# Optimization experiments

Hardware: AMD Instinct MI355X
Metric: run time of the kernel (lower is better)

Reference implementation:

```python
import jax, jax.numpy as jnp
import numpy as np

NUM_BINS = 15
BW = 0.3                      # KDE bandwidth (hard-coded in original)
VOLUME = 100.0                # (-5,5) x (-5,5) integration volume
KDE_NORM = 2.0 * np.pi * BW * BW


def _sq_dists(q, data):
    # ||q_i - d_j||^2 via the algebraic expansion (avoids [Nq, Nd, 2] blowup)
    sq = (jnp.sum(q * q, axis=1)[:, None]
          + jnp.sum(data * data, axis=1)[None, :]
          - 2.0 * q @ data.T)
    return jnp.maximum(sq, 0.0)


def kde(data, q):
    # Gaussian KDE: sum_j exp(-||q-d_j||^2 / (2 bw^2)) / (n * 2*pi*bw^2)
    k = jnp.exp(-_sq_dists(q, data) / (2.0 * BW * BW))
    return jnp.sum(k, axis=1) / (data.shape[0] * KDE_NORM)


def kde_weighted(data, q, weights, count):
    # KDE restricted to the subset selected by `weights` (0/1 mask),
    # equivalent to kde(data[weights==1], q)
    k = jnp.exp(-_sq_dists(q, data) / (2.0 * BW * BW))
    return (k @ weights) / (jnp.maximum(count, 1.0) * KDE_NORM)


def setup_inputs() -> dict:
    key = jax.random.key(0)
    ks = jax.random.split(key, 10)
    B, NTR, NTE, NMC, NCLS = 1024, 20000, 10000, 10000, 10
    return {
        "batch_train_x": jax.random.normal(ks[0], (B, 2), jnp.float32),
        "batch_train_y": jax.random.randint(ks[1], (B,), 0, NCLS),
        "train_pred": jax.random.randint(ks[2], (B,), 0, NCLS),
        "train_probs": jax.random.uniform(ks[3], (NTR,), jnp.float32),
        "test_probs": jax.random.uniform(ks[4], (NTE,), jnp.float32),
        "train_x": jax.random.normal(ks[5], (NTR, 2), jnp.float32),
        "test_x": jax.random.normal(ks[6], (NTE, 2), jnp.float32),
        "W": jax.random.normal(ks[7], (2, NCLS), jnp.float32),
        "b": jax.random.normal(ks[8], (NCLS,), jnp.float32),
        "mc_points": jax.random.uniform(ks[9], (NUM_BINS, NMC, 2), jnp.float32,
                                        minval=-5.0, maxval=5.0),
    }


def reference(batch_train_x, batch_train_y, train_pred, train_probs,
              test_probs, W, b, train_x, test_x, mc_points):
    correct = (batch_train_y == train_pred)
    cw = correct.astype(jnp.float32)          # mask defining Xset_Y_hatY
    cnt = jnp.sum(cw)
    p_y_haty = cnt / batch_train_y.shape[0]   # P(Y == hatY)

    bins = jnp.linspace(0.0, 1.0, NUM_BINS + 1)
    lowers, uppers = bins[:-1], bins[1:]

    def body(ec, inp):
        lo, hi, x = inp                                    # x: [NMC, 2]
        tr_rate = jnp.mean(((train_probs > lo) & (train_probs <= hi)).astype(jnp.float32))
        te_rate = jnp.mean(((test_probs > lo) & (test_probs <= hi)).astype(jnp.float32))

        logits = x @ W + b
        hat_s = jax.lax.stop_gradient(jnp.max(jax.nn.softmax(logits, axis=1), axis=1))
        idx = ((hat_s >= lo) & (hat_s <= hi)).astype(x.dtype)

        kde_tr = kde(train_x, x)                           # reused twice
        safe_te = jnp.where(te_rate > 0, te_rate, 1.0)
        safe_tr = jnp.where(tr_rate > 0, tr_rate, 1.0)
        d_t = jnp.where(te_rate > 0, kde(test_x, x) / safe_te, 0.0) * idx
        d_s = jnp.where(tr_rate > 0, kde_tr / safe_tr, 0.0) * idx

        p_hs = kde_weighted(batch_train_x, x, cw, cnt) * p_y_haty / (kde_tr + 1e-8)
        p_hs = jnp.clip(p_hs, 0.0, 1.0)

        integral = jnp.mean(p_hs * (d_t - d_s)) * VOLUME   # MC integration
        ec = ec + jnp.where(te_rate > 0, te_rate * jnp.abs(integral), 0.0)
        return ec, None

    ec, _ = jax.lax.scan(body, jnp.float32(0.0), (lowers, uppers, mc_points))
    return ec
```

## Files before the change

kernel.cpp:

```cpp
#include <hip/hip_runtime.h>
#include <hip/hip_bf16.h>

#define NB    15
#define NMC   10000
#define NTR   20000
#define NTE   10000
#define BSZ   1024
#define NCLS  10
#define NQ_ALL (NB * NMC)

#define KDE_NORM  0.5654866776461628f
#define EXPC      8.014972449383130f
#define TWO_EXPC  16.029944898766260f
#define LOG2E     1.4426950408889634f

#define GX      12
#define NCELL   144
#define CELL_LO -6.0f

#define MC_ST  64
#define TR_ST  224
#define TE_ST  384
#define BX_ST  544
#define MC_CUR 704
#define TR_CUR 864
#define TE_CUR 1024
#define BX_CUR 1184
#define P_PR   1344
#define PR_ZERO_FLOATS (P_PR + 3 * NQ_ALL)
#define MCS_B   (PR_ZERO_FLOATS * 4)
#define TRS_B   (MCS_B + NQ_ALL * 16)
#define TES_B   (TRS_B + NTR * 16)
#define BXS_B   (TES_B + NTE * 16)
#define PR_NEED (BXS_B + BSZ * 16)

#define QCH    7
#define SLICES 16

#define CW_OFF   64
#define P_MID    1088
#define WS_MID_FLOATS (P_MID + 3 * NQ_ALL)
#define MDS   17
#define MTILE 256
#define MMQ   8

#define WS_SMALL 1088
#define FTILE 256

typedef float v2f __attribute__((ext_vector_type(2)));

__device__ __forceinline__ float fast_exp2(float x) {
#if __has_builtin(__builtin_amdgcn_exp2f)
    return __builtin_amdgcn_exp2f(x);
#else
    return exp2f(x);
#endif
}

__device__ __forceinline__ int cell_of(float x, float y) {
    int ix = (int)floorf(x - CELL_LO);
    ix = min(max(ix, 0), GX - 1);
    int iy = (int)floorf(y - CELL_LO);
    iy = min(max(iy, 0), GX - 1);
    return iy * GX + ix;
}

__global__ __launch_bounds__(1024) void setup_count_k(
    const int* __restrict__ by, const int* __restrict__ bp,
    const float* __restrict__ trp, const float* __restrict__ tep,
    const float2* __restrict__ mc, const float2* __restrict__ tr,
    const float2* __restrict__ te, const float2* __restrict__ bx,
    float* __restrict__ ws, int* __restrict__ W)
{
    __shared__ int h[4][NCELL];
    int tid = threadIdx.x;
    for (int s = tid; s < 4 * NCELL; s += 1024) ((int*)h)[s] = 0;
    __syncthreads();

    int i    = blockIdx.x * 1024 + tid;
    int lane = tid & 63;

    float c = 0.f;
    if (i < BSZ) c = (by[i] == bp[i]) ? 1.f : 0.f;
    unsigned long long mcm = __ballot(c != 0.f);
    if (lane == 0 && mcm) atomicAdd(&ws[0], (float)__popcll(mcm));

    if ((int)blockIdx.x * 1024 < NTR) {
        float p_tr = (i < NTR) ? trp[i] : -1.f;
        float p_te = (i < NTE) ? tep[i] : -1.f;
        const float step = 1.0f / 15.0f;
        for (int b2 = 0; b2 < NB; b2++) {
            float lo = b2 * step;
            float hi = (b2 == NB - 1) ? 1.0f : (b2 + 1) * step;
            unsigned long long m1 = __ballot(p_tr > lo && p_tr <= hi);
            unsigned long long m2 = __ballot(p_te > lo && p_te <= hi);
            if (lane == 0) {
                if (m1) atomicAdd(&ws[1  + b2], (float)__popcll(m1));
                if (m2) atomicAdd(&ws[16 + b2], (float)__popcll(m2));
            }
        }
    }

    if (i < NQ_ALL) { float2 p = mc[i]; atomicAdd(&h[0][cell_of(p.x, p.y)], 1); }
    if (i < NTR)    { float2 p = tr[i]; atomicAdd(&h[1][cell_of(p.x, p.y)], 1); }
    if (i < NTE)    { float2 p = te[i]; atomicAdd(&h[2][cell_of(p.x, p.y)], 1); }
    if (i < BSZ)    { float2 p = bx[i]; atomicAdd(&h[3][cell_of(p.x, p.y)], 1); }
    __syncthreads();

    for (int s = tid; s < 4 * NCELL; s += 1024) {
        int v = ((int*)h)[s];
        if (v) {
            int ds   = s / NCELL;
            int cell = s % NCELL;
            int st   = (ds == 0) ? MC_ST : (ds == 1) ? TR_ST : (ds == 2) ? TE_ST : BX_ST;
            atomicAdd(&W[st + 1 + cell], v);
        }
    }
}

__global__ void scan_k(int* __restrict__ W)
{
    __shared__ int buf[NCELL];
    int tid = threadIdx.x;
#pragma unroll
    for (int t = 0; t < 4; ++t) {
        int st  = (t == 0) ? MC_ST  : (t == 1) ? TR_ST  : (t == 2) ? TE_ST  : BX_ST;
        int cur = (t == 0) ? MC_CUR : (t == 1) ? TR_CUR : (t == 2) ? TE_CUR : BX_CUR;
        int v = 0;
        if (tid < NCELL) { v = W[st + 1 + tid]; buf[tid] = v; }
        __syncthreads();
        for (int off = 1; off < NCELL; off <<= 1) {
            int x = 0;
            if (tid < NCELL && tid >= off) x = buf[tid - off];
            __syncthreads();
            if (tid < NCELL) buf[tid] += x;
            __syncthreads();
        }
        if (tid < NCELL) {
            int start = buf[tid] - v;
            W[st  + tid] = start;
            W[cur + tid] = start;
            if (tid == NCELL - 1) W[st + NCELL] = buf[tid];
        }
        __syncthreads();
    }
}

__global__ __launch_bounds__(1024) void scatter_priv(
    const float2* __restrict__ mc, const float2* __restrict__ tr,
    const float2* __restrict__ te, const float2* __restrict__ bx,
    const int* __restrict__ by, const int* __restrict__ bp,
    int* __restrict__ W,
    float4* __restrict__ mcS, float4* __restrict__ trS,
    float4* __restrict__ teS, float4* __restrict__ bxS)
{
    __shared__ int h[NCELL];
    __shared__ int base[NCELL];
    int ds  = blockIdx.y;
    int N   = (ds == 0) ? NQ_ALL : (ds == 1) ? NTR : (ds == 2) ? NTE : BSZ;
    if ((int)blockIdx.x * 1024 >= N) return;
    const float2* src = (ds == 0) ? mc : (ds == 1) ? tr : (ds == 2) ? te : bx;
    int cur = (ds == 0) ? MC_CUR : (ds == 1) ? TR_CUR : (ds == 2) ? TE_CUR : BX_CUR;

    int tid = threadIdx.x;
    if (tid < NCELL) h[tid] = 0;
    __syncthreads();

    int i = blockIdx.x * 1024 + tid;
    int cell = 0, rank = 0;
    float2 p;
    if (i < N) {
        p = src[i];
        cell = cell_of(p.x, p.y);
        rank = atomicAdd(&h[cell], 1);
    }
    __syncthreads();
    if (tid < NCELL && h[tid]) base[tid] = atomicAdd(&W[cur + tid], h[tid]);
    __syncthreads();

    if (i < N) {
        int pos = base[cell] + rank;
        if (ds == 0) {
            mcS[pos] = make_float4(p.x, p.y,
                                   -EXPC * fmaf(p.x, p.x, p.y * p.y),
                                   (float)(i / NMC));
        } else {
            float w = 1.f;
            if (ds == 3) w = (by[i] == bp[i]) ? 1.f : 0.f;
            float4 v = make_float4(TWO_EXPC * p.x, TWO_EXPC * p.y,
                                   -EXPC * fmaf(p.x, p.x, p.y * p.y), w);
            if (ds == 1) trS[pos] = v;
            else if (ds == 2) teS[pos] = v;
            else bxS[pos] = v;
        }
    }
}

__global__ __launch_bounds__(256) void main_k(
    const int*    __restrict__ W,
    const float4* __restrict__ mcS,
    const float4* __restrict__ trS,
    const float4* __restrict__ teS,
    const float4* __restrict__ bxS,
    float* __restrict__ P)
{
    __shared__ float4 tile[256];

    int tid   = threadIdx.x;
    int cell  = blockIdx.x;
    int chunk = blockIdx.y;
    int slice = blockIdx.z;

    int qs   = W[MC_ST + cell];
    int qend = W[MC_ST + cell + 1];
    int ci = cell % GX, cj = cell / GX;
    int dj0 = max(cj - 2, 0), dj1 = min(cj + 2, GX - 1);
    int di0 = max(ci - 2, 0), di1 = min(ci + 2, GX - 1);

    for (int q0 = qs + chunk * 256; q0 < qend; q0 += QCH * 256) {
        int  qidx  = q0 + tid;
        bool valid = qidx < qend;
        float4 q4 = mcS[valid ? qidx : qs];
        float qx = q4.x, qy = q4.y, qe = q4.z;

        float a0 = 0.f, a1 = 0.f, a2 = 0.f;
#pragma unroll
        for (int ds = 0; ds < 3; ++ds) {
            if (ds == 2 && slice != 0) continue;
            const float4* D  = (ds == 0) ? trS : ((ds == 1) ? teS : bxS);
            const int*    St = W + ((ds == 0) ? TR_ST : ((ds == 1) ? TE_ST : BX_ST));
            int ns = (ds == 2) ? 1 : SLICES;
            int sl = (ds == 2) ? 0 : slice;

            float accl = 0.f;
            for (int dj = dj0; dj <= dj1; ++dj) {
                int s0  = St[dj * GX + di0];
                int s1  = St[dj * GX + di1 + 1];
                int len = s1 - s0;
                int ss  = s0 + (len * sl) / ns;
                int se  = s0 + (len * (sl + 1)) / ns;
                for (int t0 = ss; t0 < se; t0 += 256) {
                    __syncthreads();
                    int o = t0 + tid;
                    tile[tid] = (o < se) ? D[o]
                                         : make_float4(0.f, 0.f, -1e30f, 0.f);
                    __syncthreads();
                    int cnt = min(256, se - t0);
#pragma unroll 4
                    for (int j = 0; j < cnt; ++j) {
                        float4 d = tile[j];
                        float e = fmaf(qx, d.x, fmaf(qy, d.y, d.z + qe));
                        accl = fmaf(d.w, fast_exp2(e), accl);
                    }
                }
            }
            if (ds == 0) a0 = accl; else if (ds == 1) a1 = accl; else a2 = accl;
        }

        if (valid) {
            atomicAdd(&P[qidx], a0);
            atomicAdd(&P[NQ_ALL + qidx], a1);
            if (slice == 0) atomicAdd(&P[2 * NQ_ALL + qidx], a2);
        }
        __syncthreads();
    }
}

__global__ __launch_bounds__(1024) void combine_pr(
    const float4* __restrict__ mcS,
    const float*  __restrict__ Wm,
    const float*  __restrict__ bv,
    const float*  __restrict__ wsf,
    const float*  __restrict__ P,
    float* __restrict__ S1, float* __restrict__ S2)
{
    __shared__ float sb1[NB], sb2[NB];
    int tid = threadIdx.x;
    if (tid < NB) { sb1[tid] = 0.f; sb2[tid] = 0.f; }
    __syncthreads();

#pragma unroll
    for (int rep = 0; rep < 2; ++rep) {
        int i = blockIdx.x * 2048 + rep * 1024 + tid;
        if (i < NQ_ALL) {
            float4 q4 = mcS[i];
            float qx = q4.x, qy = q4.y;
            int bin = (int)q4.w;
            float t_tr = P[i];
            float t_te = P[NQ_ALL + i];
            float t_w  = P[2 * NQ_ALL + i];

            float lmax = -1e30f;
            float l[NCLS];
#pragma unroll
            for (int c = 0; c < NCLS; ++c) {
                l[c] = fmaf(qx, Wm[c], fmaf(qy, Wm[NCLS + c], bv[c]));
                lmax = fmaxf(lmax, l[c]);
            }
            float sume = 0.f;
#pragma unroll
            for (int c = 0; c < NCLS; ++c) sume += fast_exp2((l[c] - lmax) * LOG2E);
            float hat_s = 1.0f / sume;

            const float step = 1.0f / 15.0f;
            float lo = bin * step;
            float hi = (bin == NB - 1) ? 1.0f : (bin + 1) * step;
            float ind = (hat_s >= lo && hat_s <= hi) ? 1.f : 0.f;

            float cnt    = wsf[0];
            float kde_tr = t_tr * (1.0f / (NTR * KDE_NORM));
            float kde_te = t_te * (1.0f / (NTE * KDE_NORM));
            float kw     = t_w / (fmaxf(cnt, 1.0f) * KDE_NORM);
            float p_y    = cnt * (1.0f / BSZ);
            float p_hs   = kw * p_y / (kde_tr + 1e-8f);
            p_hs = fminf(fmaxf(p_hs, 0.f), 1.f);

            float c1 = p_hs * ind * kde_te;
            float c2 = p_hs * ind * kde_tr;
            if (c1 != 0.f) atomicAdd(&sb1[bin], c1);
            if (c2 != 0.f) atomicAdd(&sb2[bin], c2);
        }
    }
    __syncthreads();
    if (tid < NB) {
        if (sb1[tid] != 0.f) atomicAdd(&S1[tid], sb1[tid]);
        if (sb2[tid] != 0.f) atomicAdd(&S2[tid], sb2[tid]);
    }
}

template <bool W>
__device__ __forceinline__ void mid_phase(const float2* __restrict__ pts,
                                          const float* __restrict__ wgt,
                                          int N, int slice,
                                          float* sAB, float* sCW,
                                          const float* qx, const float* qy, const float* qe,
                                          v2f* acc, int tid)
{
    v2f qx2[MMQ], qy2[MMQ], qe2[MMQ];
#pragma unroll
    for (int k = 0; k < MMQ; ++k) {
        qx2[k] = v2f{qx[k], qx[k]};
        qy2[k] = v2f{qy[k], qy[k]};
        qe2[k] = v2f{qe[k], qe[k]};
        acc[k] = v2f{0.f, 0.f};
    }

    int L      = (N + MDS - 1) / MDS;
    int start  = slice * L;
    int len    = min(L, N - start);
    int rounds = (len + MTILE - 1) / MTILE;
    for (int r = 0; r < rounds; ++r) {
        __syncthreads();
        int o = r * MTILE + tid;
        float a = 0.f, b = 0.f, c = -1e30f, wv = 0.f;
        if (o < len) {
            float2 p = pts[start + o];
            a = TWO_EXPC * p.x;
            b = TWO_EXPC * p.y;
            c = -EXPC * fmaf(p.x, p.x, p.y * p.y);
            if (W) wv = wgt[start + o];
        }
        int g4 = 4 * (tid >> 1) + (tid & 1);
        sAB[g4] = a;  sAB[g4 + 2] = b;
        sCW[g4] = c;  sCW[g4 + 2] = wv;
        __syncthreads();

        int cnt = min(MTILE, len - r * MTILE);
        int ng  = (cnt + 1) >> 1;
        const float4* AB4 = (const float4*)sAB;
        const float4* CW4 = (const float4*)sCW;
        for (int g = 0; g < ng; ++g) {
            float4 AB = AB4[g];
            float4 CW = CW4[g];
            v2f a01; a01.x = AB.x; a01.y = AB.y;
            v2f b01; b01.x = AB.z; b01.y = AB.w;
            v2f c01; c01.x = CW.x; c01.y = CW.y;
            v2f w01; w01.x = CW.z; w01.y = CW.w;
#pragma unroll
            for (int k = 0; k < MMQ; ++k) {
                v2f t0, t1, e;
                asm("v_pk_add_f32 %0, %1, %2" : "=v"(t0) : "v"(c01), "v"(qe2[k]));
                asm("v_pk_fma_f32 %0, %1, %2, %3" : "=v"(t1) : "v"(b01), "v"(qy2[k]), "v"(t0));
                asm("v_pk_fma_f32 %0, %1, %2, %3" : "=v"(e) : "v"(a01), "v"(qx2[k]), "v"(t1));
                float k0 = fast_exp2(e.x);
                float k1 = fast_exp2(e.y);
                if (W) {
                    acc[k].x = fmaf(w01.x, k0, acc[k].x);
                    acc[k].y = fmaf(w01.y, k1, acc[k].y);
                } else {
                    acc[k].x += k0;
                    acc[k].y += k1;
                }
            }
        }
    }
}

__global__ __launch_bounds__(256) void kdeA_mid(
    const float2* __restrict__ mc2,
    const float2* __restrict__ tr2,
    const float2* __restrict__ te2,
    const float2* __restrict__ bx2,
    const float*  __restrict__ ws,
    float* __restrict__ P)
{
    __shared__ float sAB[2 * MTILE];
    __shared__ float sCW[2 * MTILE];

    int tid   = threadIdx.x;
    int bin   = blockIdx.y;
    int slice = blockIdx.z;
    int base  = blockIdx.x * (256 * MMQ);

    int qi[MMQ];
    float qx[MMQ], qy[MMQ], qe[MMQ];
#pragma unroll
    for (int k = 0; k < MMQ; ++k) {
        qi[k] = base + k * 256 + tid;
        int qs = qi[k] < NMC ? qi[k] : (NMC - 1);
        float2 q = mc2[bin * NMC + qs];
        qx[k] = q.x;
        qy[k] = q.y;
        qe[k] = -EXPC * fmaf(q.x, q.x, q.y * q.y);
    }

    v2f acc[MMQ];

    mid_phase<false>(tr2, nullptr, NTR, slice, sAB, sCW, qx, qy, qe, acc, tid);
#pragma unroll
    for (int k = 0; k < MMQ; ++k)
        if (qi[k] < NMC) atomicAdd(&P[bin * NMC + qi[k]], acc[k].x + acc[k].y);

    mid_phase<false>(te2, nullptr, NTE, slice, sAB, sCW, qx, qy, qe, acc, tid);
#pragma unroll
    for (int k = 0; k < MMQ; ++k)
        if (qi[k] < NMC) atomicAdd(&P[NQ_ALL + bin * NMC + qi[k]], acc[k].x + acc[k].y);

    mid_phase<true>(bx2, ws + CW_OFF, BSZ, slice, sAB, sCW, qx, qy, qe, acc, tid);
#pragma unroll
    for (int k = 0; k < MMQ; ++k)
        if (qi[k] < NMC) atomicAdd(&P[2 * NQ_ALL + bin * NMC + qi[k]], acc[k].x + acc[k].y);
}

__global__ void combine_mid(const float2* __restrict__ mc2,
                            const float*  __restrict__ Wm,
                            const float*  __restrict__ bv,
                            const float*  __restrict__ ws,
                            const float*  __restrict__ P,
                            float* __restrict__ S1, float* __restrict__ S2)
{
    int bin  = blockIdx.y;
    int m    = blockIdx.x * 256 + threadIdx.x;
    int lane = threadIdx.x & 63;

    float c1 = 0.f, c2 = 0.f;
    if (m < NMC) {
        float2 q = mc2[bin * NMC + m];
        int idx  = bin * NMC + m;
        float t_tr = P[idx];
        float t_te = P[NQ_ALL + idx];
        float t_w  = P[2 * NQ_ALL + idx];

        float lmax = -1e30f;
        float l[NCLS];
#pragma unroll
        for (int c = 0; c < NCLS; ++c) {
            l[c] = fmaf(q.x, Wm[c], fmaf(q.y, Wm[NCLS + c], bv[c]));
            lmax = fmaxf(lmax, l[c]);
        }
        float sume = 0.f;
#pragma unroll
        for (int c = 0; c < NCLS; ++c) sume += expf(l[c] - lmax);
        float hat_s = 1.0f / sume;

        const float step = 1.0f / 15.0f;
        float lo = bin * step;
        float hi = (bin == NB - 1) ? 1.0f : (bin + 1) * step;
        float ind = (hat_s >= lo && hat_s <= hi) ? 1.f : 0.f;

        float cnt    = ws[0];
        float kde_tr = t_tr * (1.0f / (NTR * KDE_NORM));
        float kde_te = t_te * (1.0f / (NTE * KDE_NORM));
        float kw     = t_w / (fmaxf(cnt, 1.0f) * KDE_NORM);
        float p_y    = cnt * (1.0f / BSZ);
        float p_hs   = kw * p_y / (kde_tr + 1e-8f);
        p_hs = fminf(fmaxf(p_hs, 0.f), 1.f);

        c1 = p_hs * ind * kde_te;
        c2 = p_hs * ind * kde_tr;
    }

    for (int off = 32; off > 0; off >>= 1) {
        c1 += __shfl_down(c1, off);
        c2 += __shfl_down(c2, off);
    }
    if (lane == 0) {
        atomicAdd(&S1[bin], c1);
        atomicAdd(&S2[bin], c2);
    }
}

template <int ROUNDS, bool WEIGHTED>
__device__ __forceinline__ float kde_phase_fb(const float2* __restrict__ pts,
                                              int Nq, float4* tile,
                                              const float* __restrict__ w,
                                              int tid, int wid,
                                              float qx, float qy, float qe)
{
    float acc = 0.f;
    for (int r = 0; r < ROUNDS; ++r) {
        __syncthreads();
        int off = r * FTILE + tid;
#pragma unroll
        for (int s = 0; s < 4; ++s) {
            float4 v;
            if (off < Nq) {
                float2 p = pts[s * Nq + off];
                v.x = TWO_EXPC * p.x;
                v.y = TWO_EXPC * p.y;
                v.z = -EXPC * fmaf(p.x, p.x, p.y * p.y);
                v.w = WEIGHTED ? w[s * Nq + off] : 0.f;
            } else {
                v = make_float4(0.f, 0.f, -1e30f, 0.f);
            }
            tile[s * FTILE + tid] = v;
        }
        __syncthreads();
        const float4* t4 = &tile[wid * FTILE];
#pragma unroll 8
        for (int j = 0; j < FTILE; ++j) {
            float4 v = t4[j];
            float e = fmaf(qx, v.x, fmaf(qy, v.y, v.z)) + qe;
            float k = fast_exp2(e);
            acc = WEIGHTED ? fmaf(v.w, k, acc) : (acc + k);
        }
    }
    return acc;
}

__global__ __launch_bounds__(256) void ec_kde_fb(
    const float2* __restrict__ mc2, const float2* __restrict__ train2,
    const float2* __restrict__ test2, const float2* __restrict__ batch2,
    const float* __restrict__ Wm, const float* __restrict__ bv,
    const float* __restrict__ ws, float* __restrict__ S1, float* __restrict__ S2)
{
    __shared__ float4 tile[4 * FTILE];
    __shared__ float  red[3][256];

    int tid  = threadIdx.x;
    int wid  = tid >> 6;
    int lane = tid & 63;
    int bin  = blockIdx.y;
    int m    = blockIdx.x * 64 + lane;
    int mm   = (m < NMC) ? m : (NMC - 1);

    float2 q = mc2[bin * NMC + mm];
    float qx = q.x, qy = q.y;
    float qe = -EXPC * fmaf(qx, qx, qy * qy);

    float s_tr = kde_phase_fb<20, false>(train2, NTR / 4, tile, nullptr, tid, wid, qx, qy, qe);
    float s_te = kde_phase_fb<10, false>(test2,  NTE / 4, tile, nullptr, tid, wid, qx, qy, qe);
    float s_w  = kde_phase_fb<1,  true >(batch2, BSZ / 4, tile, ws + CW_OFF, tid, wid, qx, qy, qe);

    red[0][tid] = s_tr; red[1][tid] = s_te; red[2][tid] = s_w;
    __syncthreads();

    if (tid < 64) {
        float t_tr = ((red[0][tid] + red[0][tid + 64]) + (red[0][tid + 128] + red[0][tid + 192]));
        float t_te = ((red[1][tid] + red[1][tid + 64]) + (red[1][tid + 128] + red[1][tid + 192]));
        float t_w  = ((red[2][tid] + red[2][tid + 64]) + (red[2][tid + 128] + red[2][tid + 192]));

        float lmax = -1e30f;
        float l[NCLS];
#pragma unroll
        for (int c = 0; c < NCLS; ++c) {
            l[c] = fmaf(qx, Wm[c], fmaf(qy, Wm[NCLS + c], bv[c]));
            lmax = fmaxf(lmax, l[c]);
        }
        float sume = 0.f;
#pragma unroll
        for (int c = 0; c < NCLS; ++c) sume += expf(l[c] - lmax);
        float hat_s = 1.0f / sume;

        const float step = 1.0f / 15.0f;
        float lo = bin * step;
        float hi = (bin == NB - 1) ? 1.0f : (bin + 1) * step;
        float ind = (hat_s >= lo && hat_s <= hi) ? 1.f : 0.f;

        float cnt    = ws[0];
        float kde_tr = t_tr * (1.0f / (NTR * KDE_NORM));
        float kde_te = t_te * (1.0f / (NTE * KDE_NORM));
        float kw     = t_w / (fmaxf(cnt, 1.0f) * KDE_NORM);
        float p_y    = cnt * (1.0f / BSZ);
        float p_hs   = kw * p_y / (kde_tr + 1e-8f);
        p_hs = fminf(fmaxf(p_hs, 0.f), 1.f);

        bool valid = (m < NMC);
        float c1 = valid ? p_hs * ind * kde_te : 0.f;
        float c2 = valid ? p_hs * ind * kde_tr : 0.f;

        for (int off = 32; off > 0; off >>= 1) {
            c1 += __shfl_down(c1, off);
            c2 += __shfl_down(c2, off);
        }
        if (lane == 0) {
            atomicAdd(&S1[bin], c1);
            atomicAdd(&S2[bin], c2);
        }
    }
}

__global__ void final_k(const float* __restrict__ ws, float* __restrict__ out)
{
    if (threadIdx.x == 0 && blockIdx.x == 0) {
        float ec = 0.f;
        for (int b = 0; b < NB; ++b) {
            float tr_rate = ws[1  + b] * (1.0f / NTR);
            float te_rate = ws[16 + b] * (1.0f / NTE);
            float s1 = ws[32 + b];
            float s2 = ws[48 + b];
            float a_te = (te_rate > 0.f) ? (1.0f / te_rate) : 0.f;
            float a_tr = (tr_rate > 0.f) ? (1.0f / tr_rate) : 0.f;
            float integral = (a_te * s1 - a_tr * s2) * (1.0f / NMC) * 100.0f;
            if (te_rate > 0.f) ec += te_rate * fabsf(integral);
        }
        out[0] = ec;
    }
}

extern "C" void kernel_launch(void* const* d_in, const int* in_sizes, int n_in,
                              void* d_out, int out_size, void* d_ws, size_t ws_size,
                              hipStream_t stream)
{
    const float* batch_x = (const float*)d_in[0];
    const int*   by      = (const int*)  d_in[1];
    const int*   bp      = (const int*)  d_in[2];
    const float* trp     = (const float*)d_in[3];
    const float* tep     = (const float*)d_in[4];
    const float* train_x = (const float*)d_in[5];
    const float* test_x  = (const float*)d_in[6];
    const float* Wm      = (const float*)d_in[7];
    const float* bv      = (const float*)d_in[8];
    const float* mc      = (const float*)d_in[9];

    float* ws  = (float*)d_ws;
    float* out = (float*)d_out;

    if (ws_size >= (size_t)PR_NEED) {
        hipMemsetAsync(d_ws, 0, (size_t)PR_ZERO_FLOATS * sizeof(float), stream);

        int*    W   = (int*)d_ws;
        float4* mcS = (float4*)((char*)d_ws + MCS_B);
        float4* trS = (float4*)((char*)d_ws + TRS_B);
        float4* teS = (float4*)((char*)d_ws + TES_B);
        float4* bxS = (float4*)((char*)d_ws + BXS_B);

        int nblk = (NQ_ALL + 1023) / 1024;
        setup_count_k<<<nblk, 1024, 0, stream>>>(
            by, bp, trp, tep,
            (const float2*)mc, (const float2*)train_x,
            (const float2*)test_x, (const float2*)batch_x, ws, W);

        scan_k<<<1, 256, 0, stream>>>(W);

        dim3 gsc(nblk, 4);
        scatter_priv<<<gsc, 1024, 0, stream>>>(
            (const float2*)mc, (const float2*)train_x,
            (const float2*)test_x, (const float2*)batch_x,
            by, bp, W, mcS, trS, teS, bxS);

        dim3 grid(NCELL, QCH, SLICES);
        main_k<<<grid, 256, 0, stream>>>(W, mcS, trS, teS, bxS, ws + P_PR);

        combine_pr<<<(NQ_ALL + 2047) / 2048, 1024, 0, stream>>>(
            mcS, Wm, bv, ws, ws + P_PR, ws + 32, ws + 48);
    } else if (ws_size >= (size_t)WS_MID_FLOATS * sizeof(float)) {
        hipMemsetAsync(d_ws, 0, (size_t)WS_MID_FLOATS * sizeof(float), stream);

        int nthr = 256;
        {
        }
        extern __global__ void setup_mid_k(const int*, const int*, const float*,
                                           const float*, float*);
        setup_mid_k<<<(NTR + nthr - 1) / nthr, nthr, 0, stream>>>(by, bp, trp, tep, ws);

        dim3 gA((NMC + 256 * MMQ - 1) / (256 * MMQ), NB, MDS);
        kdeA_mid<<<gA, 256, 0, stream>>>(
            (const float2*)mc, (const float2*)train_x, (const float2*)test_x,
            (const float2*)batch_x, ws, ws + P_MID);

        dim3 gB((NMC + 255) / 256, NB);
        combine_mid<<<gB, 256, 0, stream>>>(
            (const float2*)mc, Wm, bv, ws, ws + P_MID, ws + 32, ws + 48);
    } else {
        hipMemsetAsync(d_ws, 0, WS_SMALL * sizeof(float), stream);

        extern __global__ void setup_mid_k(const int*, const int*, const float*,
                                           const float*, float*);
        setup_mid_k<<<(NTR + 255) / 256, 256, 0, stream>>>(by, bp, trp, tep, ws);

        dim3 grid((NMC + 63) / 64, NB);
        ec_kde_fb<<<grid, 256, 0, stream>>>(
            (const float2*)mc,
            (const float2*)train_x, (const float2*)test_x, (const float2*)batch_x,
            Wm, bv, ws, ws + 32, ws + 48);
    }

    final_k<<<1, 64, 0, stream>>>(ws, out);
}

__global__ void setup_mid_k(const int* __restrict__ by, const int* __restrict__ bp,
                            const float* __restrict__ trp, const float* __restrict__ tep,
                            float* __restrict__ ws)
{
    int i    = blockIdx.x * blockDim.x + threadIdx.x;
    int lane = threadIdx.x & 63;

    float c = 0.f;
    if (i < BSZ) {
        c = (by[i] == bp[i]) ? 1.f : 0.f;
        ws[CW_OFF + i] = c;
    }
    unsigned long long mc = __ballot(c != 0.f);
    if (lane == 0 && mc) atomicAdd(&ws[0], (float)__popcll(mc));

    float p_tr = (i < NTR) ? trp[i] : -1.f;
    float p_te = (i < NTE) ? tep[i] : -1.f;
    const float step = 1.0f / 15.0f;
    for (int b2 = 0; b2 < NB; b2++) {
        float lo = b2 * step;
        float hi = (b2 == NB - 1) ? 1.0f : (b2 + 1) * step;
        unsigned long long m1 = __ballot(p_tr > lo && p_tr <= hi);
        unsigned long long m2 = __ballot(p_te > lo && p_te <= hi);
        if (lane == 0) {
            if (m1) atomicAdd(&ws[1  + b2], (float)__popcll(m1));
            if (m2) atomicAdd(&ws[16 + b2], (float)__popcll(m2));
        }
    }
}
```

Before: 381.8 us.

## Compute two queries per thread in main KDE kernel with cell-centered exponent offset

Each thread in main_k now handles two query points, so every shared-memory data tile is reused for twice the queries, and the chunk count drops from 7 to 3 to fit. The per-query exponent offset is replaced by a per-cell constant folded into the staged data, and the true offset is reapplied as one exp2 scale at the end. This saves an add per pair and a third of the barrier and tile-load work per query. The cost is more registers and fewer blocks, and shifting the offset to the cell centre could change the range the exponentials underflow or overflow in.

```diff
diff --git a/kernel.cpp b/kernel.cpp
--- a/kernel.cpp
+++ b/kernel.cpp
@@ -34,7 +34,7 @@
 #define BXS_B   (TES_B + NTE * 16)
 #define PR_NEED (BXS_B + BSZ * 16)
 
-#define QCH    7
+#define QCH    3
 #define SLICES 16
 
 #define CW_OFF   64
@@ -64,6 +64,10 @@
     iy = min(max(iy, 0), GX - 1);
     return iy * GX + ix;
 }
+
+__global__ void setup_mid_k(const int* __restrict__ by, const int* __restrict__ bp,
+                            const float* __restrict__ trp, const float* __restrict__ tep,
+                            float* __restrict__ ws);
 
 __global__ __launch_bounds__(1024) void setup_count_k(
     const int* __restrict__ by, const int* __restrict__ bp,
@@ -214,16 +218,21 @@
     int qs   = W[MC_ST + cell];
     int qend = W[MC_ST + cell + 1];
     int ci = cell % GX, cj = cell / GX;
+    float cx = CELL_LO + ci + 0.5f;
+    float cy = CELL_LO + cj + 0.5f;
+    float KC = -EXPC * fmaf(cx, cx, cy * cy);
     int dj0 = max(cj - 2, 0), dj1 = min(cj + 2, GX - 1);
     int di0 = max(ci - 2, 0), di1 = min(ci + 2, GX - 1);
 
-    for (int q0 = qs + chunk * 256; q0 < qend; q0 += QCH * 256) {
-        int  qidx  = q0 + tid;
-        bool valid = qidx < qend;
-        float4 q4 = mcS[valid ? qidx : qs];
-        float qx = q4.x, qy = q4.y, qe = q4.z;
+    for (int q0 = qs + chunk * 512; q0 < qend; q0 += QCH * 512) {
+        int  qa = q0 + tid;
+        int  qb = q0 + 256 + tid;
+        bool va = qa < qend, vb = qb < qend;
+        float4 A = mcS[va ? qa : qs];
+        float4 B = mcS[vb ? qb : qs];
 
         float a0 = 0.f, a1 = 0.f, a2 = 0.f;
+        float b0 = 0.f, b1 = 0.f, b2 = 0.f;
 #pragma unroll
         for (int ds = 0; ds < 3; ++ds) {
             if (ds == 2 && slice != 0) continue;
@@ -232,7 +241,7 @@
             int ns = (ds == 2) ? 1 : SLICES;
             int sl = (ds == 2) ? 0 : slice;
 
-            float accl = 0.f;
+            float accA = 0.f, accB = 0.f;
             for (int dj = dj0; dj <= dj1; ++dj) {
                 int s0  = St[dj * GX + di0];
                 int s1  = St[dj * GX + di1 + 1];
@@ -242,25 +251,41 @@
                 for (int t0 = ss; t0 < se; t0 += 256) {
                     __syncthreads();
                     int o = t0 + tid;
-                    tile[tid] = (o < se) ? D[o]
-                                         : make_float4(0.f, 0.f, -1e30f, 0.f);
+                    if (o < se) {
+                        float4 v = D[o];
+                        v.z += KC;
+                        tile[tid] = v;
+                    } else {
+                        tile[tid] = make_float4(0.f, 0.f, -1e30f, 0.f);
+                    }
                     __syncthreads();
                     int cnt = min(256, se - t0);
 #pragma unroll 4
                     for (int j = 0; j < cnt; ++j) {
                         float4 d = tile[j];
-                        float e = fmaf(qx, d.x, fmaf(qy, d.y, d.z + qe));
-                        accl = fmaf(d.w, fast_exp2(e), accl);
+                        float ea = fmaf(A.x, d.x, fmaf(A.y, d.y, d.z));
+                        float eb = fmaf(B.x, d.x, fmaf(B.y, d.y, d.z));
+                        accA = fmaf(d.w, fast_exp2(ea), accA);
+                        accB = fmaf(d.w, fast_exp2(eb), accB);
                     }
                 }
             }
-            if (ds == 0) a0 = accl; else if (ds == 1) a1 = accl; else a2 = accl;
-        }
-
-        if (valid) {
-            atomicAdd(&P[qidx], a0);
-            atomicAdd(&P[NQ_ALL + qidx], a1);
-            if (slice == 0) atomicAdd(&P[2 * NQ_ALL + qidx], a2);
+            if (ds == 0)      { a0 = accA; b0 = accB; }
+            else if (ds == 1) { a1 = accA; b1 = accB; }
+            else              { a2 = accA; b2 = accB; }
+        }
+
+        if (va) {
+            float s = fast_exp2(A.z - KC);
+            atomicAdd(&P[qa], a0 * s);
+            atomicAdd(&P[NQ_ALL + qa], a1 * s);
+            if (slice == 0) atomicAdd(&P[2 * NQ_ALL + qa], a2 * s);
+        }
+        if (vb) {
+            float s = fast_exp2(B.z - KC);
+            atomicAdd(&P[qb], b0 * s);
+            atomicAdd(&P[NQ_ALL + qb], b1 * s);
+            if (slice == 0) atomicAdd(&P[2 * NQ_ALL + qb], b2 * s);
         }
         __syncthreads();
     }
@@ -677,12 +702,7 @@
     } else if (ws_size >= (size_t)WS_MID_FLOATS * sizeof(float)) {
         hipMemsetAsync(d_ws, 0, (size_t)WS_MID_FLOATS * sizeof(float), stream);
 
-        int nthr = 256;
-        {
-        }
-        extern __global__ void setup_mid_k(const int*, const int*, const float*,
-                                           const float*, float*);
-        setup_mid_k<<<(NTR + nthr - 1) / nthr, nthr, 0, stream>>>(by, bp, trp, tep, ws);
+        setup_mid_k<<<(NTR + 255) / 256, 256, 0, stream>>>(by, bp, trp, tep, ws);
 
         dim3 gA((NMC + 256 * MMQ - 1) / (256 * MMQ), NB, MDS);
         kdeA_mid<<<gA, 256, 0, stream>>>(
@@ -695,8 +715,6 @@
     } else {
         hipMemsetAsync(d_ws, 0, WS_SMALL * sizeof(float), stream);
 
-        extern __global__ void setup_mid_k(const int*, const int*, const float*,
-                                           const float*, float*);
         setup_mid_k<<<(NTR + 255) / 256, 256, 0, stream>>>(by, bp, trp, tep, ws);
 
         dim3 grid((NMC + 63) / 64, NB);
```

Result: slower. 436.9 us (+14.4%).
